# Optimization experiments

Hardware: AMD Instinct MI355X
Metric: run time of the kernel (lower is better)

## Reference

```python
import jax, jax.numpy as jnp
import numpy as np

B, T, D = 8, 4096, 1024
N_EXPERTS, N_SLOTS = 64, 8
HID = 256


def setup_inputs() -> dict:
    key = jax.random.key(0)
    ks = jax.random.split(key, 8)
    s = lambda *sh: 1.0 / np.sqrt(sh[-2]) if len(sh) >= 2 else 0.02
    tokens = jax.random.normal(ks[0], (B, T, D), dtype=jnp.float32)
    # routing weights, original uses np.random.random -> uniform [0,1); scale down for stability
    expert_mixture = jax.random.uniform(ks[1], (D, N_EXPERTS * N_SLOTS), dtype=jnp.float32) * 0.02
    W1 = jax.random.normal(ks[2], (N_EXPERTS, D, HID), dtype=jnp.float32) / np.sqrt(D)
    b1 = jnp.zeros((N_EXPERTS, HID), dtype=jnp.float32)
    W2 = jax.random.normal(ks[3], (N_EXPERTS, HID, HID), dtype=jnp.float32) / np.sqrt(HID)
    b2 = jnp.zeros((N_EXPERTS, HID), dtype=jnp.float32)
    W3 = jax.random.normal(ks[4], (N_EXPERTS, HID, D), dtype=jnp.float32) / np.sqrt(HID)
    b3 = jnp.zeros((N_EXPERTS, D), dtype=jnp.float32)
    return {"tokens": tokens, "expert_mixture": expert_mixture,
            "W1": W1, "b1": b1, "W2": W2, "b2": b2, "W3": W3, "b3": b3}


def reference(tokens, expert_mixture, W1, b1, W2, b2, W3, b3):
    b, t, d = tokens.shape
    flat = tokens.reshape(-1, d)                       # [BT, D]
    mat = flat @ expert_mixture                        # [BT, n*p]
    row_probs = jax.nn.softmax(mat, axis=0)            # over tokens
    col_probs = jax.nn.softmax(mat, axis=1)            # over slots
    x_hat = row_probs.T @ flat                         # [n*p, D] dispatch
    xs = x_hat.reshape(N_EXPERTS, N_SLOTS, d)          # [n, p, D]
    # per-expert MLP: Linear-ReLU-Linear-ReLU-Linear (batched over experts)
    h = jax.nn.relu(jnp.einsum('npd,ndh->nph', xs, W1) + b1[:, None, :])
    h = jax.nn.relu(jnp.einsum('nph,nhk->npk', h, W2) + b2[:, None, :])
    y_hat = jnp.einsum('npk,nkd->npd', h, W3) + b3[:, None, :]
    y_hat = y_hat.reshape(N_EXPERTS * N_SLOTS, d)      # [n*p, D]
    y = col_probs @ y_hat                              # [BT, D] combine
    return y.reshape(b, t, d)
```

## Files before the change

kernel.cpp:

```cpp
#include <hip/hip_runtime.h>
#include <math.h>

namespace {

constexpr int BT  = 8 * 4096;
constexpr int DIM = 1024;
constexpr int NE  = 64;
constexpr int NS  = 8;
constexpr int NP  = NE * NS;
constexpr int HID = 256;

typedef float f32x4 __attribute__((ext_vector_type(4)));
typedef __bf16 bf16x8 __attribute__((ext_vector_type(8)));
typedef short s16x8 __attribute__((ext_vector_type(8)));

__device__ __forceinline__ ushort f2bf(float x) {
  union { float f; unsigned u; } a; a.f = x;
  unsigned r = a.u + 0x7FFFu + ((a.u >> 16) & 1u);
  return (ushort)(r >> 16);
}
__device__ __forceinline__ float bf2f(ushort u) {
  union { unsigned u; float f; } a; a.u = (unsigned)u << 16;
  return a.f;
}

__device__ __forceinline__ void gload16(const void* g, void* l) {
  __builtin_amdgcn_global_load_lds(
      (const __attribute__((address_space(1))) void*)g,
      (__attribute__((address_space(3))) void*)l, 16, 0, 0);
}

template <bool ATOMIC, bool OBF, bool CSTAT>
__global__ __launch_bounds__(512) void k_gemm(const ushort* __restrict__ A,
                                              const ushort* __restrict__ Bt,
                                              void* __restrict__ Cv,
                                              int N, int kchunk,
                                              int lda, int ldb,
                                              float* __restrict__ pmOut,
                                              float* __restrict__ pzOut,
                                              float* __restrict__ rpmOut,
                                              float* __restrict__ rpzOut) {
  __shared__ __align__(16) ushort As0[256 * 64];
  __shared__ __align__(16) ushort As1[256 * 64];
  __shared__ __align__(16) ushort As2[256 * 64];
  __shared__ __align__(16) ushort Bs0[128 * 64];
  __shared__ __align__(16) ushort Bs1[128 * 64];
  __shared__ __align__(16) ushort Bs2[128 * 64];

  const int tid = threadIdx.x;
  const int wid = tid >> 6;
  const int lane = tid & 63;

  const int gx = gridDim.x, gy = gridDim.y;
  int wg = (blockIdx.z * gy + blockIdx.y) * gx + blockIdx.x;
  const int nwg = gx * gy * gridDim.z;
  wg = (wg & 7) * (nwg >> 3) + (wg >> 3);
  const int bx = wg % gx;
  const int rest = wg / gx;
  const int by = rest % gy;
  const int bz = rest / gy;

  const int n0 = bx * 128;
  const int m0 = by * 256;
  const int kb = bz * kchunk;

  const int w8 = wid * 8;
  const int lr = lane >> 3;
  const int ks = (((lane & 7) ^ lr) * 8);
  const ushort* Asrc = A + (size_t)(m0 + w8 + lr) * lda + ks;
  const ushort* Bsrc = Bt + (size_t)(n0 + w8 + lr) * ldb + ks;

  const int wm64 = (wid >> 1) * 64;
  const int wn64 = (wid & 1) * 64;
  const int fr = lane & 15;
  const int fq = lane >> 4;
  const int fq8 = fq * 8;
  const int frsw = (fr & 7) << 3;

  f32x4 acc[4][4];
#pragma unroll
  for (int i = 0; i < 4; ++i)
#pragma unroll
    for (int j = 0; j < 4; ++j) acc[i][j] = (f32x4){0.f, 0.f, 0.f, 0.f};

  const int nt = kchunk / 64;

#define STAGE6(An_, Bn_, kt_)                                                    \
  do {                                                                           \
    _Pragma("unroll") for (int q = 0; q < 4; ++q)                                \
      gload16(Asrc + (size_t)(q * 64) * lda + (kt_), (An_) + (q * 64 + w8) * 64);\
    _Pragma("unroll") for (int q = 0; q < 2; ++q)                                \
      gload16(Bsrc + (size_t)(q * 64) * ldb + (kt_), (Bn_) + (q * 64 + w8) * 64);\
  } while (0)

#define LD(B_, r_, h_)                                                          \
  __builtin_bit_cast(bf16x8, *(const s16x8*)((B_) + (size_t)(r_) * 64 +         \
                                             (((h_) * 32 + fq8) ^ frsw)))

#define GBLOCK(Ab_, Bb_, An_, Bn_, tt_)                                         \
  do {                                                                          \
    if ((tt_) + 1 < nt) asm volatile("s_waitcnt vmcnt(6)" ::: "memory");        \
    else                asm volatile("s_waitcnt vmcnt(0)" ::: "memory");        \
    __builtin_amdgcn_sched_barrier(0);                                          \
    __builtin_amdgcn_s_barrier();                                               \
    __builtin_amdgcn_sched_barrier(0);                                          \
    if ((tt_) + 2 < nt) STAGE6(An_, Bn_, kb + ((tt_) + 2) * 64);                \
    bf16x8 bfr_[4][2];                                                          \
    _Pragma("unroll") for (int n = 0; n < 4; ++n) {                             \
      bfr_[n][0] = LD(Bb_, wn64 + n * 16 + fr, 0);                              \
      bfr_[n][1] = LD(Bb_, wn64 + n * 16 + fr, 1);                              \
    }                                                                           \
    _Pragma("unroll") for (int m = 0; m < 4; ++m) {                             \
      bf16x8 a0_ = LD(Ab_, wm64 + m * 16 + fr, 0);                              \
      bf16x8 a1_ = LD(Ab_, wm64 + m * 16 + fr, 1);                              \
      __builtin_amdgcn_s_setprio(1);                                            \
      _Pragma("unroll") for (int n = 0; n < 4; ++n)                             \
        acc[m][n] = __builtin_amdgcn_mfma_f32_16x16x32_bf16(a0_, bfr_[n][0],    \
                                                            acc[m][n], 0, 0, 0);\
      _Pragma("unroll") for (int n = 0; n < 4; ++n)                             \
        acc[m][n] = __builtin_amdgcn_mfma_f32_16x16x32_bf16(a1_, bfr_[n][1],    \
                                                            acc[m][n], 0, 0, 0);\
      __builtin_amdgcn_s_setprio(0);                                            \
    }                                                                           \
  } while (0)

  STAGE6(As0, Bs0, kb);
  STAGE6(As1, Bs1, kb + 64);
  int t = 0;
  for (; t + 3 <= nt; t += 3) {
    GBLOCK(As0, Bs0, As2, Bs2, t);
    GBLOCK(As1, Bs1, As0, Bs0, t + 1);
    GBLOCK(As2, Bs2, As1, Bs1, t + 2);
  }
  if (t < nt) { GBLOCK(As0, Bs0, As2, Bs2, t); ++t; }
  if (t < nt) { GBLOCK(As1, Bs1, As0, Bs0, t); ++t; }
#undef GBLOCK
#undef LD
#undef STAGE6

  if (OBF) {
    ushort* Cb = (ushort*)Cv + (size_t)(m0 + wm64 + fq * 4) * N + n0 + wn64 + fr;
#pragma unroll
    for (int m = 0; m < 4; ++m)
#pragma unroll
      for (int n = 0; n < 4; ++n)
#pragma unroll
        for (int r = 0; r < 4; ++r)
          Cb[(size_t)(m * 16 + r) * N + n * 16] = f2bf(acc[m][n][r]);
  } else {
    float* Cb = (float*)Cv + (size_t)(m0 + wm64 + fq * 4) * N + n0 + wn64 + fr;
#pragma unroll
    for (int m = 0; m < 4; ++m)
#pragma unroll
      for (int n = 0; n < 4; ++n)
#pragma unroll
        for (int r = 0; r < 4; ++r) {
          float* p = Cb + (size_t)(m * 16 + r) * N + n * 16;
          if (ATOMIC) atomicAdd(p, acc[m][n][r]);
          else *p = acc[m][n][r];
        }
  }

  if (CSTAT) {
    float cm_[4], cz_[4];
#pragma unroll
    for (int n = 0; n < 4; ++n) { cm_[n] = -INFINITY; cz_[n] = 0.f; }
#pragma unroll
    for (int m = 0; m < 4; ++m)
#pragma unroll
      for (int n = 0; n < 4; ++n)
#pragma unroll
        for (int r = 0; r < 4; ++r) {
          float v = acc[m][n][r];
          float mm = fmaxf(cm_[n], v);
          cz_[n] = cz_[n] * __expf(cm_[n] - mm) + __expf(v - mm);
          cm_[n] = mm;
        }
#pragma unroll
    for (int off = 16; off <= 32; off <<= 1)
#pragma unroll
      for (int n = 0; n < 4; ++n) {
        float m2 = __shfl_xor(cm_[n], off);
        float z2 = __shfl_xor(cz_[n], off);
        float mm = fmaxf(cm_[n], m2);
        cz_[n] = cz_[n] * __expf(cm_[n] - mm) + z2 * __expf(m2 - mm);
        cm_[n] = mm;
      }
    float rm_[16], rz_[16];
#pragma unroll
    for (int m = 0; m < 4; ++m)
#pragma unroll
      for (int r = 0; r < 4; ++r) {
        const int i = m * 4 + r;
        float mx = fmaxf(fmaxf(acc[m][0][r], acc[m][1][r]),
                         fmaxf(acc[m][2][r], acc[m][3][r]));
        rm_[i] = mx;
        rz_[i] = __expf(acc[m][0][r] - mx) + __expf(acc[m][1][r] - mx) +
                 __expf(acc[m][2][r] - mx) + __expf(acc[m][3][r] - mx);
      }
#pragma unroll
    for (int off = 1; off <= 8; off <<= 1)
#pragma unroll
      for (int i = 0; i < 16; ++i) {
        float m2 = __shfl_xor(rm_[i], off);
        float z2 = __shfl_xor(rz_[i], off);
        float mm = fmaxf(rm_[i], m2);
        rz_[i] = rz_[i] * __expf(rm_[i] - mm) + z2 * __expf(m2 - mm);
        rm_[i] = mm;
      }
    __syncthreads();
    float* smx = (float*)As0;
    float* smz = smx + 4 * 128;
    float* smr = (float*)Bs0;
    float* smz2 = smr + 512;
    const int mrow = wid >> 1;
    if (lane < 16) {
#pragma unroll
      for (int n = 0; n < 4; ++n) {
        smx[mrow * 128 + wn64 + n * 16 + lane] = cm_[n];
        smz[mrow * 128 + wn64 + n * 16 + lane] = cz_[n];
      }
    }
    if (fr == 0) {
#pragma unroll
      for (int m = 0; m < 4; ++m)
#pragma unroll
        for (int r = 0; r < 4; ++r) {
          const int row = wm64 + m * 16 + fq * 4 + r;
          smr[(wid & 1) * 256 + row] = rm_[m * 4 + r];
          smz2[(wid & 1) * 256 + row] = rz_[m * 4 + r];
        }
    }
    __syncthreads();
    if (tid < 128) {
      float m = smx[tid], z = smz[tid];
#pragma unroll
      for (int p = 1; p < 4; ++p) {
        float m2 = smx[p * 128 + tid], z2 = smz[p * 128 + tid];
        float mm = fmaxf(m, m2);
        z = z * __expf(m - mm) + z2 * __expf(m2 - mm);
        m = mm;
      }
      pmOut[(size_t)by * NP + n0 + tid] = m;
      pzOut[(size_t)by * NP + n0 + tid] = z;
    }
    if (tid < 256) {
      float m1 = smr[tid], z1 = smz2[tid];
      float m2 = smr[256 + tid], z2 = smz2[256 + tid];
      float mm = fmaxf(m1, m2);
      float zz = z1 * __expf(m1 - mm) + z2 * __expf(m2 - mm);
      rpmOut[(size_t)bx * BT + m0 + tid] = mm;
      rpzOut[(size_t)bx * BT + m0 + tid] = zz;
    }
  }
}

__global__ __launch_bounds__(256) void k_prep(const float* __restrict__ tokens,
                                              const float* __restrict__ em,
                                              const float* __restrict__ b1,
                                              const float* __restrict__ b2,
                                              const float* __restrict__ b3,
                                              ushort* __restrict__ tokens_bf,
                                              ushort* __restrict__ emT,
                                              float* __restrict__ base) {
  __shared__ __align__(16) ushort tT[64][256];
  const int tid = threadIdx.x;
  const int bid = blockIdx.x;
  if (bid < 2048) {
    const size_t n = (size_t)BT * DIM;
    size_t i = ((size_t)bid * 256 + tid) * 8;
    const size_t stride = (size_t)2048 * 256 * 8;
    for (; i < n; i += stride) {
      float4 a = *(const float4*)(tokens + i);
      float4 b = *(const float4*)(tokens + i + 4);
      s16x8 o;
      o[0] = (short)f2bf(a.x); o[1] = (short)f2bf(a.y);
      o[2] = (short)f2bf(a.z); o[3] = (short)f2bf(a.w);
      o[4] = (short)f2bf(b.x); o[5] = (short)f2bf(b.y);
      o[6] = (short)f2bf(b.z); o[7] = (short)f2bf(b.w);
      *(s16x8*)(tokens_bf + i) = o;
    }
  } else if (bid < 2080) {
    const int b = bid - 2048;
    const int r0 = (b >> 3) * 256, c0 = (b & 7) * 64;
#pragma unroll
    for (int i = 0; i < 16; ++i) {
      const int idx = i * 256 + tid;
      const int r = idx >> 4, c4 = (idx & 15) * 4;
      float4 v = *(const float4*)(em + (size_t)(r0 + r) * NP + c0 + c4);
      ushort u[4] = {f2bf(v.x), f2bf(v.y), f2bf(v.z), f2bf(v.w)};
#pragma unroll
      for (int j = 0; j < 4; ++j)
        tT[c4 + j][r ^ (((c4 + j) & 7) << 3)] = u[j];
    }
    __syncthreads();
#pragma unroll
    for (int i = 0; i < 8; ++i) {
      const int idx = i * 256 + tid;
      const int c = idx >> 5, r8 = (idx & 31) * 8;
      s16x8 o = *(const s16x8*)&tT[c][r8 ^ ((c & 7) << 3)];
      *(s16x8*)(emT + (size_t)(c0 + c) * DIM + r0 + r8) = o;
    }
  } else {
    constexpr size_t XH = (size_t)NP * DIM;
    constexpr size_t H1 = (size_t)NP * HID;
    constexpr size_t TOT4 = (2 * XH + 2 * H1) / 4;
    size_t i = (size_t)(bid - 2080) * 256 + tid;
    for (; i < TOT4; i += (size_t)1024 * 256) {
      const size_t idx = i * 4;
      float4 v;
      if (idx < XH) {
        v = make_float4(0.f, 0.f, 0.f, 0.f);
      } else if (idx < XH + H1) {
        const size_t k = idx - XH;
        v = *(const float4*)(b1 + (k / HID) / NS * HID + k % HID);
      } else if (idx < XH + 2 * H1) {
        const size_t k = idx - XH - H1;
        v = *(const float4*)(b2 + (k / HID) / NS * HID + k % HID);
      } else {
        const size_t k = idx - XH - 2 * H1;
        v = *(const float4*)(b3 + (k / DIM) / NS * DIM + k % DIM);
      }
      *(float4*)(base + idx) = v;
    }
  }
}

__global__ __launch_bounds__(256) void k_tpose(const ushort* __restrict__ X,
                                               ushort* __restrict__ Yt,
                                               int Cc, int ldt) {
  __shared__ __align__(16) ushort tT[64][256];
  const int tid = threadIdx.x;
  const int r0 = blockIdx.x * 256, c0 = blockIdx.y * 64;
#pragma unroll
  for (int i = 0; i < 8; ++i) {
    const int idx = i * 256 + tid;
    const int r = idx >> 3, c8 = (idx & 7) * 8;
    s16x8 v = *(const s16x8*)(X + (size_t)(r0 + r) * Cc + c0 + c8);
#pragma unroll
    for (int j = 0; j < 8; ++j)
      tT[c8 + j][r ^ (((c8 + j) & 7) << 3)] = (ushort)v[j];
  }
  __syncthreads();
#pragma unroll
  for (int i = 0; i < 8; ++i) {
    const int idx = i * 256 + tid;
    const int c = idx >> 5, r8 = (idx & 31) * 8;
    s16x8 o = *(const s16x8*)&tT[c][r8 ^ ((c & 7) << 3)];
    *(s16x8*)(Yt + (size_t)(c0 + c) * ldt + r0 + r8) = o;
  }
}

__global__ __launch_bounds__(256) void k_cvtT(const float* __restrict__ X,
                                              ushort* __restrict__ Yt,
                                              int Cc, int ldt) {
  __shared__ __align__(16) ushort tT[64][256];
  const int tid = threadIdx.x;
  const int r0 = blockIdx.x * 256, c0 = blockIdx.y * 64;
#pragma unroll
  for (int i = 0; i < 16; ++i) {
    const int idx = i * 256 + tid;
    const int r = idx >> 4, c4 = (idx & 15) * 4;
    float4 v = *(const float4*)(X + (size_t)(r0 + r) * Cc + c0 + c4);
    ushort u[4] = {f2bf(v.x), f2bf(v.y), f2bf(v.z), f2bf(v.w)};
#pragma unroll
    for (int j = 0; j < 4; ++j)
      tT[c4 + j][r ^ (((c4 + j) & 7) << 3)] = u[j];
  }
  __syncthreads();
#pragma unroll
  for (int i = 0; i < 8; ++i) {
    const int idx = i * 256 + tid;
    const int c = idx >> 5, r8 = (idx & 31) * 8;
    s16x8 o = *(const s16x8*)&tT[c][r8 ^ ((c & 7) << 3)];
    *(s16x8*)(Yt + (size_t)(c0 + c) * ldt + r0 + r8) = o;
  }
}

__global__ __launch_bounds__(256) void k_probs2(const ushort* __restrict__ mat,
                                                const float* __restrict__ pm,
                                                const float* __restrict__ pz,
                                                const float* __restrict__ rpm,
                                                const float* __restrict__ rpz,
                                                ushort* __restrict__ Pc,
                                                ushort* __restrict__ Pt) {
  __shared__ __align__(16) ushort tT[64][256];
  __shared__ float s0buf[64], s1buf[64];
  __shared__ float sm[4][64], sz[4][64];
  const int tid = threadIdx.x;
  const int bid = blockIdx.x;
  if (bid < BT / 64) {
    const int t0 = bid * 64;
    if (tid < 64) {
      const int t = t0 + tid;
      float m = -INFINITY, z = 0.f;
#pragma unroll
      for (int c = 0; c < 4; ++c) {
        float m2 = rpm[(size_t)c * BT + t], z2 = rpz[(size_t)c * BT + t];
        float mm = fmaxf(m, m2);
        z = z * __expf(m - mm) + z2 * __expf(m2 - mm);
        m = mm;
      }
      s0buf[tid] = m;
      s1buf[tid] = 1.f / z;
    }
    __syncthreads();
#pragma unroll
    for (int i = 0; i < 16; ++i) {
      const int idx = i * 256 + tid;
      const int r = idx >> 6, c8 = (idx & 63) * 8;
      s16x8 v = *(const s16x8*)(mat + (size_t)(t0 + r) * NP + c8);
      const float mr = s0buf[r], zr = s1buf[r];
      s16x8 oc;
#pragma unroll
      for (int j = 0; j < 8; ++j)
        oc[j] = (short)f2bf(__expf(bf2f((ushort)v[j]) - mr) * zr);
      *(s16x8*)(Pc + (size_t)(t0 + r) * NP + c8) = oc;
    }
  } else {
    const int b2 = bid - BT / 64;
    const int t0 = (b2 % (BT / 256)) * 256, s0 = (b2 / (BT / 256)) * 64;
    {
      const int col = s0 + (tid & 63);
      const int q = tid >> 6;
      float m = -INFINITY, z = 0.f;
      for (int r = q; r < BT / 256; r += 4) {
        float m2 = pm[(size_t)r * NP + col], z2 = pz[(size_t)r * NP + col];
        float mm = fmaxf(m, m2);
        z = z * __expf(m - mm) + z2 * __expf(m2 - mm);
        m = mm;
      }
      sm[q][tid & 63] = m;
      sz[q][tid & 63] = z;
    }
    __syncthreads();
    if (tid < 64) {
      float m = sm[0][tid], z = sz[0][tid];
#pragma unroll
      for (int p = 1; p < 4; ++p) {
        float m2 = sm[p][tid], z2 = sz[p][tid];
        float mm = fmaxf(m, m2);
        z = z * __expf(m - mm) + z2 * __expf(m2 - mm);
        m = mm;
      }
      s0buf[tid] = m;
      s1buf[tid] = 1.f / z;
    }
    __syncthreads();
#pragma unroll
    for (int i = 0; i < 8; ++i) {
      const int idx = i * 256 + tid;
      const int r = idx >> 3, c8 = (idx & 7) * 8;
      s16x8 v = *(const s16x8*)(mat + (size_t)(t0 + r) * NP + s0 + c8);
#pragma unroll
      for (int j = 0; j < 8; ++j)
        tT[c8 + j][r ^ (((c8 + j) & 7) << 3)] =
            f2bf(__expf(bf2f((ushort)v[j]) - s0buf[c8 + j]) * s1buf[c8 + j]);
    }
    __syncthreads();
#pragma unroll
    for (int i = 0; i < 8; ++i) {
      const int idx = i * 256 + tid;
      const int c = idx >> 5, r8 = (idx & 31) * 8;
      s16x8 o = *(const s16x8*)&tT[c][r8 ^ ((c & 7) << 3)];
      *(s16x8*)(Pt + (size_t)(s0 + c) * BT + t0 + r8) = o;
    }
  }
}

template <int K, int N, int KS, bool RELU_IN>
__global__ __launch_bounds__(256) void k_mlp(const float* __restrict__ X,
                                             const float* __restrict__ W,
                                             float* __restrict__ Y) {
  constexpr int KSL = K / KS;
  __shared__ float xs[NS * KSL];
  const int tid = threadIdx.x;
  const int e = blockIdx.x;
  const int k0 = blockIdx.z * KSL;
  constexpr int T4 = (NS * KSL) / 4;
  for (int i = tid; i < T4; i += 256) {
    const int p = i / (KSL / 4), kk4 = (i % (KSL / 4)) * 4;
    float4 v = *(const float4*)(X + (size_t)(e * NS + p) * K + k0 + kk4);
    if (RELU_IN) {
      v.x = fmaxf(v.x, 0.f); v.y = fmaxf(v.y, 0.f);
      v.z = fmaxf(v.z, 0.f); v.w = fmaxf(v.w, 0.f);
    }
    *(float4*)(xs + p * KSL + kk4) = v;
  }
  __syncthreads();
  const int j = blockIdx.y * 64 + (tid & 63);
  const int pr = tid >> 6;
  const float* w = W + (size_t)e * K * N + (size_t)k0 * N + j;
  const float* x0 = xs + pr * KSL;
  const float* x1 = xs + (pr + 4) * KSL;
  float a0 = 0.f, a1 = 0.f;
#pragma unroll 8
  for (int k = 0; k < KSL; ++k) {
    float wv = w[(size_t)k * N];
    a0 += x0[k] * wv;
    a1 += x1[k] * wv;
  }
  atomicAdd(Y + (size_t)(e * NS + pr) * N + j, a0);
  atomicAdd(Y + (size_t)(e * NS + pr + 4) * N + j, a1);
}

}

extern "C" void kernel_launch(void* const* d_in, const int* in_sizes, int n_in,
                              void* d_out, int out_size, void* d_ws, size_t ws_size,
                              hipStream_t stream) {
  const float* tokens = (const float*)d_in[0];
  const float* em     = (const float*)d_in[1];
  const float* W1     = (const float*)d_in[2];
  const float* b1     = (const float*)d_in[3];
  const float* W2     = (const float*)d_in[4];
  const float* b2     = (const float*)d_in[5];
  const float* W3     = (const float*)d_in[6];
  const float* b3     = (const float*)d_in[7];
  float* out = (float*)d_out;

  char* w = (char*)d_ws;
  ushort* matb      = (ushort*)w; w += (size_t)BT * NP * 2;
  ushort* tokens_bf = (ushort*)w; w += (size_t)BT * DIM * 2;
  ushort* tokT      = (ushort*)w; w += (size_t)DIM * BT * 2;
  ushort* Pt        = (ushort*)w; w += (size_t)NP * BT * 2;
  ushort* Pc        = (ushort*)w; w += (size_t)BT * NP * 2;
  ushort* emT       = (ushort*)w; w += (size_t)NP * DIM * 2;
  ushort* yhatT     = (ushort*)w; w += (size_t)DIM * NP * 2;
  float*  pm        = (float*)w;  w += (size_t)(BT / 256) * NP * 4;
  float*  pz        = (float*)w;  w += (size_t)(BT / 256) * NP * 4;
  float*  rpm       = (float*)w;  w += (size_t)4 * BT * 4;
  float*  rpz       = (float*)w;  w += (size_t)4 * BT * 4;
  float*  xhat      = (float*)w;  w += (size_t)NP * DIM * 4;
  float*  h1        = (float*)w;  w += (size_t)NP * HID * 4;
  float*  h2        = (float*)w;  w += (size_t)NP * HID * 4;
  float*  yhat      = (float*)w;  w += (size_t)NP * DIM * 4;
  (void)ws_size; (void)in_sizes; (void)n_in; (void)out_size;

  k_prep<<<3104, 256, 0, stream>>>(tokens, em, b1, b2, b3, tokens_bf, emT, xhat);
  k_tpose<<<dim3(BT / 256, DIM / 64), 256, 0, stream>>>(tokens_bf, tokT, DIM, BT);
  k_gemm<false, true, true><<<dim3(NP / 128, BT / 256, 1), 512, 0, stream>>>(
      tokens_bf, emT, matb, NP, DIM, DIM, DIM, pm, pz, rpm, rpz);
  k_probs2<<<BT / 64 + (BT / 256) * (NP / 64), 256, 0, stream>>>(
      matb, pm, pz, rpm, rpz, Pc, Pt);
  k_gemm<true, false, false><<<dim3(DIM / 128, NP / 256, 16), 512, 0, stream>>>(
      Pt, tokT, xhat, DIM, BT / 16, BT, BT, nullptr, nullptr, nullptr, nullptr);
  k_mlp<DIM, HID, 8, false><<<dim3(NE, HID / 64, 8), 256, 0, stream>>>(xhat, W1, h1);
  k_mlp<HID, HID, 4, true><<<dim3(NE, HID / 64, 4), 256, 0, stream>>>(h1, W2, h2);
  k_mlp<HID, DIM, 4, true><<<dim3(NE, DIM / 64, 4), 256, 0, stream>>>(h2, W3, yhat);
  k_cvtT<<<dim3(NP / 256, DIM / 64), 256, 0, stream>>>(yhat, yhatT, DIM, NP);
  k_gemm<false, false, false><<<dim3(DIM / 128, BT / 256, 1), 512, 0, stream>>>(
      Pc, yhatT, out, DIM, NP, NP, NP, nullptr, nullptr, nullptr, nullptr);
}
```

Baseline: 323.6 us.

## Add dedicated 128x128 double-buffered GEMM for the combine step

```diff
diff --git a/kernel.cpp b/kernel.cpp
--- a/kernel.cpp
+++ b/kernel.cpp
@@ -135,7 +135,6 @@
   if (t < nt) { GBLOCK(As0, Bs0, As2, Bs2, t); ++t; }
   if (t < nt) { GBLOCK(As1, Bs1, As0, Bs0, t); ++t; }
 #undef GBLOCK
-#undef LD
 #undef STAGE6
 
   if (OBF) {
@@ -253,6 +252,112 @@
       rpzOut[(size_t)bx * BT + m0 + tid] = zz;
     }
   }
+#undef LD
+}
+
+__global__ __launch_bounds__(512) void k_gemmC(const ushort* __restrict__ A,
+                                               const ushort* __restrict__ Bt,
+                                               float* __restrict__ C,
+                                               int N, int K) {
+  __shared__ __align__(16) ushort As0[128 * 64];
+  __shared__ __align__(16) ushort Bs0[128 * 64];
+  __shared__ __align__(16) ushort As1[128 * 64];
+  __shared__ __align__(16) ushort Bs1[128 * 64];
+  const int tid = threadIdx.x;
+  const int wid = tid >> 6;
+  const int lane = tid & 63;
+
+  const int gx = gridDim.x, gy = gridDim.y;
+  int wg = blockIdx.y * gx + blockIdx.x;
+  const int nwg = gx * gy;
+  wg = (wg & 7) * (nwg >> 3) + (wg >> 3);
+  const int bx = wg % gx;
+  const int by = wg / gx;
+  const int n0 = bx * 128;
+  const int m0 = by * 128;
+
+  const int w8 = wid * 8;
+  const int lr = lane >> 3;
+  const int ks = ((lane & 7) ^ lr) * 8;
+  const ushort* Asrc = A + (size_t)(m0 + w8 + lr) * K + ks;
+  const ushort* Bsrc = Bt + (size_t)(n0 + w8 + lr) * K + ks;
+
+  const int wm64 = (wid >> 2) * 64;
+  const int wn32 = (wid & 3) * 32;
+  const int fr = lane & 15;
+  const int fq = lane >> 4;
+  const int fq8 = fq * 8;
+  const int frsw = (fr & 7) << 3;
+
+  f32x4 acc[4][2];
+#pragma unroll
+  for (int i = 0; i < 4; ++i)
+#pragma unroll
+    for (int j = 0; j < 2; ++j) acc[i][j] = (f32x4){0.f, 0.f, 0.f, 0.f};
+
+  const int nt = K / 64;
+
+#define CSTAGE(An_, Bn_, kt_)                                                   \
+  do {                                                                          \
+    _Pragma("unroll") for (int q = 0; q < 2; ++q)                               \
+      gload16(Asrc + (size_t)(q * 64) * K + (kt_), (An_) + (q * 64 + w8) * 64); \
+    _Pragma("unroll") for (int q = 0; q < 2; ++q)                               \
+      gload16(Bsrc + (size_t)(q * 64) * K + (kt_), (Bn_) + (q * 64 + w8) * 64); \
+  } while (0)
+
+#define CLD(B_, r_, h_)                                                         \
+  __builtin_bit_cast(bf16x8, *(const s16x8*)((B_) + (size_t)(r_) * 64 +         \
+                                             (((h_) * 32 + fq8) ^ frsw)))
+
+#define CITER(Ab_, Bb_, An_, Bn_, tt_)                                          \
+  do {                                                                          \
+    if ((tt_) + 1 < nt) {                                                       \
+      CSTAGE(An_, Bn_, ((tt_) + 1) * 64);                                       \
+      asm volatile("s_waitcnt vmcnt(4)" ::: "memory");                          \
+    } else {                                                                    \
+      asm volatile("s_waitcnt vmcnt(0)" ::: "memory");                          \
+    }                                                                           \
+    __builtin_amdgcn_sched_barrier(0);                                          \
+    __builtin_amdgcn_s_barrier();                                               \
+    __builtin_amdgcn_sched_barrier(0);                                          \
+    bf16x8 b_[2][2];                                                            \
+    _Pragma("unroll") for (int n = 0; n < 2; ++n) {                             \
+      b_[n][0] = CLD(Bb_, wn32 + n * 16 + fr, 0);                               \
+      b_[n][1] = CLD(Bb_, wn32 + n * 16 + fr, 1);                               \
+    }                                                                           \
+    _Pragma("unroll") for (int m = 0; m < 4; ++m) {                             \
+      bf16x8 a0_ = CLD(Ab_, wm64 + m * 16 + fr, 0);                             \
+      bf16x8 a1_ = CLD(Ab_, wm64 + m * 16 + fr, 1);                             \
+      __builtin_amdgcn_s_setprio(1);                                            \
+      _Pragma("unroll") for (int n = 0; n < 2; ++n)                             \
+        acc[m][n] = __builtin_amdgcn_mfma_f32_16x16x32_bf16(a0_, b_[n][0],      \
+                                                            acc[m][n], 0, 0, 0);\
+      _Pragma("unroll") for (int n = 0; n < 2; ++n)                             \
+        acc[m][n] = __builtin_amdgcn_mfma_f32_16x16x32_bf16(a1_, b_[n][1],      \
+                                                            acc[m][n], 0, 0, 0);\
+      __builtin_amdgcn_s_setprio(0);                                            \
+    }                                                                           \
+    __builtin_amdgcn_sched_barrier(0);                                          \
+    __builtin_amdgcn_s_barrier();                                               \
+  } while (0)
+
+  CSTAGE(As0, Bs0, 0);
+  for (int t = 0; t < nt; t += 2) {
+    CITER(As0, Bs0, As1, Bs1, t);
+    CITER(As1, Bs1, As0, Bs0, t + 1);
+  }
+#undef CITER
+#undef CLD
+#undef CSTAGE
+
+  float* Cb = C + (size_t)(m0 + wm64 + fq * 4) * N + n0 + wn32 + fr;
+#pragma unroll
+  for (int m = 0; m < 4; ++m)
+#pragma unroll
+    for (int n = 0; n < 2; ++n)
+#pragma unroll
+      for (int r = 0; r < 4; ++r)
+        Cb[(size_t)(m * 16 + r) * N + n * 16] = acc[m][n][r];
 }
 
 __global__ __launch_bounds__(256) void k_prep(const float* __restrict__ tokens,
@@ -549,6 +654,5 @@
   k_mlp<HID, HID, 4, true><<<dim3(NE, HID / 64, 4), 256, 0, stream>>>(h1, W2, h2);
   k_mlp<HID, DIM, 4, true><<<dim3(NE, DIM / 64, 4), 256, 0, stream>>>(h2, W3, yhat);
   k_cvtT<<<dim3(NP / 256, DIM / 64), 256, 0, stream>>>(yhat, yhatT, DIM, NP);
-  k_gemm<false, false, false><<<dim3(DIM / 128, BT / 256, 1), 512, 0, stream>>>(
-      Pc, yhatT, out, DIM, NP, NP, NP, nullptr, nullptr, nullptr, nullptr);
-}
+  k_gemmC<<<dim3(DIM / 128, BT / 128), 512, 0, stream>>>(Pc, yhatT, out, DIM, NP);
+}
```

After: 325.3 us. Within noise of the previous version (+0.5%).
